# Optimization experiments

Measured on AMD Instinct MI355X. Metric: run time of the kernel, lower is better.

The kernel has to match this reference:

```python
import jax, jax.numpy as jnp
import numpy as np

B, N, H, A, O = 32, 1024, 256, 32, 256
RESAMPLE_THRESHOLD = 0.5
EPS = 1e-10


def setup_inputs() -> dict:
    key = jax.random.key(0)
    ks = jax.random.split(key, 16)
    s = 0.05  # small weight scale (stands in for xavier init, keeps softmax sane)
    w = jax.random.uniform(ks[1], (B, N), jnp.float32)
    return {
        "particles": jax.random.normal(ks[0], (B, N, H), jnp.float32),
        "weights": w / jnp.sum(w, axis=1, keepdims=True),
        "action": jax.random.normal(ks[2], (B, A), jnp.float32),
        "observation": jax.random.normal(ks[3], (B, O), jnp.float32),
        "u": jax.random.uniform(ks[4], (B, 1), jnp.float32),
        "Wr": jax.random.normal(ks[5], (H + A, H), jnp.float32) * s,
        "br": jnp.zeros((H,), jnp.float32),
        "Wu": jax.random.normal(ks[6], (H + A, H), jnp.float32) * s,
        "bu": jnp.zeros((H,), jnp.float32),
        "Wc": jax.random.normal(ks[7], (H + A, H), jnp.float32) * s,
        "bc": jnp.zeros((H,), jnp.float32),
        "W0": jax.random.normal(ks[8], (H + O, H), jnp.float32) * s,
        "b0": jnp.zeros((H,), jnp.float32),
        "W1": jax.random.normal(ks[9], (H, H), jnp.float32) * s,
        "b1": jnp.zeros((H,), jnp.float32),
        "W2": jax.random.normal(ks[10], (H, 1), jnp.float32) * s,
        "b2": jnp.zeros((1,), jnp.float32),
    }


def reference(particles, weights, action, observation, u,
              Wr, br, Wu, bu, Wc, bc, W0, b0, W1, b1, W2, b2):
    b, n, h = particles.shape
    act = jnp.broadcast_to(action[:, None, :], (b, n, action.shape[-1]))
    obs = jnp.broadcast_to(observation[:, None, :], (b, n, observation.shape[-1]))

    # --- GRU-style transition (stochastic head is dead code in update()) ---
    x = jnp.concatenate([particles, act], axis=-1)            # [B,N,H+A]
    reset = jax.nn.sigmoid(x @ Wr + br)
    update = jax.nn.sigmoid(x @ Wu + bu)
    x_reset = jnp.concatenate([particles * reset, act], axis=-1)
    cand = jnp.tanh(x_reset @ Wc + bc)
    nxt = (1.0 - update) * particles + update * cand          # [B,N,H]

    # --- observation log-likelihood MLP ---
    z = jnp.concatenate([nxt, obs], axis=-1)                  # [B,N,H+O]
    z = jax.nn.gelu(z @ W0 + b0, approximate=False)
    z = jax.nn.gelu(z @ W1 + b1, approximate=False)
    log_lik = (z @ W2 + b2)[..., 0]                           # [B,N]

    # --- weight update (stable softmax) ---
    log_w = jnp.log(weights + EPS) + log_lik
    log_w = log_w - jnp.max(log_w, axis=1, keepdims=True)
    new_w = jax.nn.softmax(log_w, axis=1)                     # [B,N]

    ess = 1.0 / (jnp.sum(new_w * new_w, axis=1) + EPS)        # [B]
    should = ess < RESAMPLE_THRESHOLD * n                     # [B] bool

    # --- systematic resampling (computed for all rows, selected by mask) ---
    csum = jnp.cumsum(new_w, axis=1)                          # [B,N]
    pos = u / n + jnp.arange(n, dtype=jnp.float32) / n        # [B,N]
    pos = jnp.minimum(pos, 0.9999)
    idx = jax.vmap(jnp.searchsorted)(csum, pos)               # [B,N]
    idx = jnp.clip(idx, 0, n - 1)
    resampled = jnp.take_along_axis(nxt, idx[..., None], axis=1)
    uniform_w = jnp.full_like(new_w, 1.0 / n)

    nxt = jnp.where(should[:, None, None], resampled, nxt)
    new_w = jnp.where(should[:, None], uniform_w, new_w)

    belief = jnp.sum(nxt * new_w[..., None], axis=1)          # [B,H]
    return belief, nxt, new_w, ess
```

## Files before the change

### kernel.cpp

```cpp
#include <hip/hip_runtime.h>
#include <math.h>

#define B_ 32
#define N_ 1024
#define H_ 256
#define A_ 32
#define O_ 256
#define M_ (B_*N_)
#define EPSF 1e-10f

typedef _Float16 f16;
typedef __attribute__((ext_vector_type(8))) _Float16 f16x8;
typedef __attribute__((ext_vector_type(4))) _Float16 f16x4;
typedef __attribute__((ext_vector_type(2))) _Float16 f16x2;
typedef __attribute__((ext_vector_type(4))) float    f32x4;

__device__ __forceinline__ float gelu_exact(float x){
  return 0.5f * x * (1.0f + erff(x * 0.70710678118654752f));
}
__device__ __forceinline__ float sigm(float x){
  return 1.0f / (1.0f + expf(-x));
}

__global__ __launch_bounds__(256) void k_prep(
    const float* __restrict__ action, const float* __restrict__ observation,
    const float* __restrict__ Wr, const float* __restrict__ br,
    const float* __restrict__ Wu, const float* __restrict__ bu,
    const float* __restrict__ Wc, const float* __restrict__ bc,
    const float* __restrict__ W0, const float* __restrict__ b0,
    f16* __restrict__ WrT, f16* __restrict__ WuT, f16* __restrict__ WcT,
    f16* __restrict__ W0T, f16* __restrict__ W1T, const float* __restrict__ W1,
    float* __restrict__ actR, float* __restrict__ actU,
    float* __restrict__ actC, float* __restrict__ obs0)
{
  const int blk = blockIdx.x;
  if (blk < 80) {
    __shared__ float tile[64][65];
    const int mat = blk >> 4;
    const int kb  = ((blk & 15) >> 2) * 64;
    const int nb  = (blk & 3) * 64;
    const float* W; f16* WT;
    switch (mat) {
      case 0: W = Wr; WT = WrT; break;
      case 1: W = Wu; WT = WuT; break;
      case 2: W = Wc; WT = WcT; break;
      case 3: W = W0; WT = W0T; break;
      default: W = W1; WT = W1T; break;
    }
    const int t = threadIdx.x;
    const int c = t & 63, r4 = t >> 6;
    #pragma unroll
    for (int i = 0; i < 64; i += 4)
      tile[i + r4][c] = W[(size_t)(kb + i + r4)*H_ + nb + c];
    __syncthreads();
    #pragma unroll
    for (int i = 0; i < 64; i += 4)
      WT[(size_t)(nb + i + r4)*H_ + kb + c] = (f16)tile[c][i + r4];
  } else {
    const int b = blk - 80, j = threadIdx.x;
    float aR = br[j], aU = bu[j], aC = bc[j];
    for (int a = 0; a < A_; ++a) {
      float av = action[b*A_ + a];
      aR = fmaf(av, Wr[(H_+a)*H_ + j], aR);
      aU = fmaf(av, Wu[(H_+a)*H_ + j], aU);
      aC = fmaf(av, Wc[(H_+a)*H_ + j], aC);
    }
    float o0 = b0[j];
    for (int o = 0; o < O_; ++o)
      o0 = fmaf(observation[b*O_ + o], W0[(H_+o)*H_ + j], o0);
    actR[b*H_+j] = aR; actU[b*H_+j] = aU; actC[b*H_+j] = aC; obs0[b*H_+j] = o0;
  }
}

__device__ __forceinline__ f16x8 lda(const unsigned char* xs, int m, int kt,
                                     int lr, int lg) {
  int row = m*16 + lr;
  int off = (row*512 + kt*64 + lg*16) ^ ((row&7)<<4);
  return *(const f16x8*)(xs + off);
}
__device__ __forceinline__ f16 xs_r16(const unsigned char* xs, int row, int col) {
  int off = (row*512 + col*2) ^ ((row&7)<<4);
  return *(const f16*)(xs + off);
}
__device__ __forceinline__ void xs_w16(unsigned char* xs, int row, int col, f16 v) {
  int off = (row*512 + col*2) ^ ((row&7)<<4);
  *(f16*)(xs + off) = v;
}

__device__ __forceinline__ void gemm256(const unsigned char* xs, const f16* __restrict__ Wt,
                                        int lr, int lg, int colbase,
                                        f32x4 acc[4][4]) {
  for (int kt = 0; kt < 8; ++kt) {
    f16x8 a[4];
    #pragma unroll
    for (int m = 0; m < 4; ++m) a[m] = lda(xs, m, kt, lr, lg);
    #pragma unroll
    for (int n = 0; n < 4; ++n) {
      f16x8 bb = *(const f16x8*)(Wt + (size_t)(colbase + n*16 + lr)*H_ + kt*32 + lg*8);
      #pragma unroll
      for (int m = 0; m < 4; ++m)
        acc[m][n] = __builtin_amdgcn_mfma_f32_16x16x32_f16(a[m], bb, acc[m][n], 0, 0, 0);
    }
  }
}

__global__ __launch_bounds__(256, 2) void k_gru_mlp(
    const float* __restrict__ particles, const float* __restrict__ weights,
    const f16* __restrict__ WrT, const f16* __restrict__ WuT,
    const f16* __restrict__ WcT, const f16* __restrict__ W0T,
    const f16* __restrict__ W1T,
    const float* __restrict__ W2, const float* __restrict__ b1v,
    const float* __restrict__ b2v,
    const float* __restrict__ actR, const float* __restrict__ actU,
    const float* __restrict__ actC, const float* __restrict__ obs0,
    f16* __restrict__ ws_nxt16, float* __restrict__ log_w)
{
  __shared__ __align__(16) unsigned char xs[64*512];
  __shared__ float red[4][64];

  const int b    = blockIdx.x >> 4;
  const int n0   = (blockIdx.x & 15) << 6;
  const int tid  = threadIdx.x;
  const int w    = tid >> 6;
  const int lane = tid & 63;
  const int lr   = lane & 15;
  const int lg   = lane >> 4;
  const int colbase = w << 6;
  const float* Pbase = particles + (size_t)(b*N_ + n0) * H_;

  int colv[4];
  #pragma unroll
  for (int n = 0; n < 4; ++n) colv[n] = colbase + n*16 + lr;

  #pragma unroll
  for (int i = 0; i < 8; ++i) {
    int s = tid + i*256;
    int row = s >> 5, ks = s & 31;
    const float* src = Pbase + row*H_ + ks*8;
    float4 v0 = *(const float4*)src;
    float4 v1 = *(const float4*)(src + 4);
    f16x8 h;
    h[0]=(f16)v0.x; h[1]=(f16)v0.y; h[2]=(f16)v0.z; h[3]=(f16)v0.w;
    h[4]=(f16)v1.x; h[5]=(f16)v1.y; h[6]=(f16)v1.z; h[7]=(f16)v1.w;
    int off = (row*512 + ks*16) ^ ((row&7)<<4);
    *(f16x8*)(xs + off) = h;
  }
  __syncthreads();

  f32x4 aR[4][4];
  #pragma unroll
  for (int m=0;m<4;++m)
    #pragma unroll
    for (int n=0;n<4;++n) aR[m][n] = (f32x4)(0.f);
  gemm256(xs, WrT, lr, lg, colbase, aR);

  f32x4 aU[4][4];
  #pragma unroll
  for (int m=0;m<4;++m)
    #pragma unroll
    for (int n=0;n<4;++n) aU[m][n] = (f32x4)(0.f);
  gemm256(xs, WuT, lr, lg, colbase, aU);

  float vR[4], vU[4];
  #pragma unroll
  for (int n=0;n<4;++n) { vR[n] = actR[b*H_ + colv[n]]; vU[n] = actU[b*H_ + colv[n]]; }

  f16x4 uh[4][4];
  #pragma unroll
  for (int m=0;m<4;++m)
    #pragma unroll
    for (int n=0;n<4;++n)
      #pragma unroll
      for (int r=0;r<4;++r) {
        aR[m][n][r] = sigm(aR[m][n][r] + vR[n]);
        uh[m][n][r] = (f16)sigm(aU[m][n][r] + vU[n]);
      }

  __syncthreads();

  f16x4 oh[4][4];
  #pragma unroll
  for (int m=0;m<4;++m)
    #pragma unroll
    for (int n=0;n<4;++n)
      #pragma unroll
      for (int r=0;r<4;++r) {
        int row = m*16 + lg*4 + r;
        f16 o = xs_r16(xs, row, colv[n]);
        oh[m][n][r] = o;
        xs_w16(xs, row, colv[n], (f16)((float)o * aR[m][n][r]));
      }
  __syncthreads();

  f32x4 aC[4][4];
  #pragma unroll
  for (int m=0;m<4;++m)
    #pragma unroll
    for (int n=0;n<4;++n) aC[m][n] = (f32x4)(0.f);
  gemm256(xs, WcT, lr, lg, colbase, aC);

  float vC[4];
  #pragma unroll
  for (int n=0;n<4;++n) vC[n] = actC[b*H_ + colv[n]];

  __syncthreads();
  #pragma unroll
  for (int m=0;m<4;++m)
    #pragma unroll
    for (int n=0;n<4;++n)
      #pragma unroll
      for (int r=0;r<4;++r) {
        int row = m*16 + lg*4 + r;
        float cand = tanhf(aC[m][n][r] + vC[n]);
        float orig = (float)oh[m][n][r];
        float nx   = fmaf((float)uh[m][n][r], cand - orig, orig);
        xs_w16(xs, row, colv[n], (f16)nx);
      }
  __syncthreads();

  f16* wsrow = ws_nxt16 + (size_t)(b*N_ + n0) * H_;
  #pragma unroll
  for (int i = 0; i < 8; ++i) {
    int s = tid + i*256;
    int row = s >> 5, c16 = s & 31;
    int off = (row*512 + c16*16) ^ ((row&7)<<4);
    f16x8 v = *(const f16x8*)(xs + off);
    *(f16x8*)(wsrow + row*H_ + c16*8) = v;
  }

  f32x4 a0[4][4];
  #pragma unroll
  for (int m=0;m<4;++m)
    #pragma unroll
    for (int n=0;n<4;++n) a0[m][n] = (f32x4)(0.f);
  gemm256(xs, W0T, lr, lg, colbase, a0);

  float v0b[4];
  #pragma unroll
  for (int n=0;n<4;++n) v0b[n] = obs0[b*H_ + colv[n]];
  #pragma unroll
  for (int m=0;m<4;++m)
    #pragma unroll
    for (int n=0;n<4;++n)
      #pragma unroll
      for (int r=0;r<4;++r)
        a0[m][n][r] = gelu_exact(a0[m][n][r] + v0b[n]);
  __syncthreads();
  #pragma unroll
  for (int m=0;m<4;++m)
    #pragma unroll
    for (int n=0;n<4;++n)
      #pragma unroll
      for (int r=0;r<4;++r)
        xs_w16(xs, m*16 + lg*4 + r, colv[n], (f16)a0[m][n][r]);
  __syncthreads();

  f32x4 a1[4][4];
  #pragma unroll
  for (int m=0;m<4;++m)
    #pragma unroll
    for (int n=0;n<4;++n) a1[m][n] = (f32x4)(0.f);
  gemm256(xs, W1T, lr, lg, colbase, a1);

  float v1b[4], w2v[4];
  #pragma unroll
  for (int n=0;n<4;++n) { v1b[n] = b1v[colv[n]]; w2v[n] = W2[colv[n]]; }

  float psum[4][4];
  #pragma unroll
  for (int m=0;m<4;++m)
    #pragma unroll
    for (int r=0;r<4;++r) psum[m][r] = 0.f;
  #pragma unroll
  for (int m=0;m<4;++m)
    #pragma unroll
    for (int n=0;n<4;++n)
      #pragma unroll
      for (int r=0;r<4;++r)
        psum[m][r] = fmaf(gelu_exact(a1[m][n][r] + v1b[n]), w2v[n], psum[m][r]);

  #pragma unroll
  for (int m=0;m<4;++m)
    #pragma unroll
    for (int r=0;r<4;++r) {
      float v = psum[m][r];
      v += __shfl_xor(v, 1); v += __shfl_xor(v, 2);
      v += __shfl_xor(v, 4); v += __shfl_xor(v, 8);
      psum[m][r] = v;
    }
  if (lr == 0) {
    #pragma unroll
    for (int m=0;m<4;++m)
      #pragma unroll
      for (int r=0;r<4;++r)
        red[w][m*16 + lg*4 + r] = psum[m][r];
  }
  __syncthreads();
  if (tid < 64) {
    float ll = red[0][tid] + red[1][tid] + red[2][tid] + red[3][tid] + b2v[0];
    int gi = b*N_ + n0 + tid;
    log_w[gi] = logf(weights[gi] + EPSF) + ll;
  }
}

__global__ __launch_bounds__(256) void k_softmax(
    const float* __restrict__ log_w, const float* __restrict__ u_in,
    float* __restrict__ d_new_w, float* __restrict__ d_ess,
    int* __restrict__ ws_idx, float* __restrict__ ws_should)
{
  __shared__ float cs[N_];
  __shared__ float redbuf[4];
  __shared__ float wsum[4];
  const int b = blockIdx.x, t = threadIdx.x;
  const int wave = t >> 6, lane = t & 63;
  const float* lw = log_w + b*N_;

  float v[4];
  float m = -INFINITY;
  #pragma unroll
  for (int q = 0; q < 4; ++q) { v[q] = lw[t*4+q]; m = fmaxf(m, v[q]); }
  for (int off = 32; off >= 1; off >>= 1) m = fmaxf(m, __shfl_xor(m, off));
  if (lane == 0) redbuf[wave] = m;
  __syncthreads();
  m = fmaxf(fmaxf(redbuf[0], redbuf[1]), fmaxf(redbuf[2], redbuf[3]));

  float s4 = 0.f;
  #pragma unroll
  for (int q = 0; q < 4; ++q) { v[q] = expf(v[q] - m); s4 += v[q]; }

  float incl = s4;
  #pragma unroll
  for (int off = 1; off < 64; off <<= 1) {
    float t2 = __shfl_up(incl, off);
    if (lane >= off) incl += t2;
  }
  if (lane == 63) wsum[wave] = incl;
  __syncthreads();
  float woff = 0.f;
  #pragma unroll
  for (int ww = 0; ww < 4; ++ww) woff += (ww < wave) ? wsum[ww] : 0.f;
  const float total = wsum[0] + wsum[1] + wsum[2] + wsum[3];
  const float excl  = woff + incl - s4;
  const float inv   = 1.0f / total;

  float run = excl, sq4 = 0.f;
  #pragma unroll
  for (int q = 0; q < 4; ++q) {
    run += v[q];
    cs[t*4+q] = run * inv;
    float wq = v[q] * inv;
    sq4 += wq * wq;
  }
  for (int off = 32; off >= 1; off >>= 1) sq4 += __shfl_xor(sq4, off);
  __syncthreads();
  if (lane == 0) redbuf[wave] = sq4;
  __syncthreads();
  const float ssq = redbuf[0] + redbuf[1] + redbuf[2] + redbuf[3];
  const float ess = 1.0f / (ssq + EPSF);
  const bool should = ess < (0.5f * (float)N_);
  if (t == 0) { d_ess[b] = ess; ws_should[b] = should ? 1.0f : 0.0f; }

  const float uw = 1.0f / (float)N_;
  #pragma unroll
  for (int q = 0; q < 4; ++q)
    d_new_w[b*N_ + t*4+q] = should ? uw : v[q] * inv;

  const float ub = u_in[b];
  #pragma unroll
  for (int q = 0; q < 4; ++q) {
    int i = t*4 + q;
    float pos = fminf(ub / (float)N_ + (float)i / (float)N_, 0.9999f);
    int lo = 0, hi = N_;
    while (lo < hi) { int mid = (lo + hi) >> 1; if (cs[mid] < pos) lo = mid + 1; else hi = mid; }
    ws_idx[b*N_ + i] = (lo < N_-1) ? lo : N_-1;
  }
}

__global__ __launch_bounds__(256) void k_final(
    const f16* __restrict__ ws_nxt16, const int* __restrict__ ws_idx,
    const float* __restrict__ ws_should, const float* __restrict__ d_new_w,
    float* __restrict__ d_nxt, float* __restrict__ d_belief)
{
  const int blk = blockIdx.x;
  const int b   = blk >> 4;
  const int n0  = (blk & 15) << 6;
  const int t   = threadIdx.x;
  const int c   = t & 127;
  const int hf  = t >> 7;
  const bool should = ws_should[b] != 0.0f;
  float p0 = 0.f, p1 = 0.f;
  #pragma unroll 4
  for (int r = 0; r < 32; ++r) {
    int n = n0 + hf*32 + r;
    int src = should ? ws_idx[b*N_ + n] : n;
    f16x2 v = *(const f16x2*)(ws_nxt16 + (size_t)(b*N_ + src)*H_ + c*2);
    float w = d_new_w[b*N_ + n];
    float2 st; st.x = (float)v[0]; st.y = (float)v[1];
    *(float2*)(d_nxt + (size_t)(b*N_ + n)*H_ + c*2) = st;
    p0 = fmaf(st.x, w, p0); p1 = fmaf(st.y, w, p1);
  }
  atomicAdd(&d_belief[b*H_ + c*2],     p0);
  atomicAdd(&d_belief[b*H_ + c*2 + 1], p1);
}

extern "C" void kernel_launch(void* const* d_in, const int* in_sizes, int n_in,
                              void* d_out, int out_size, void* d_ws, size_t ws_size,
                              hipStream_t stream) {
  (void)in_sizes; (void)n_in; (void)out_size; (void)ws_size;
  const float* particles   = (const float*)d_in[0];
  const float* weights     = (const float*)d_in[1];
  const float* action      = (const float*)d_in[2];
  const float* observation = (const float*)d_in[3];
  const float* u_in        = (const float*)d_in[4];
  const float* Wr = (const float*)d_in[5];
  const float* br = (const float*)d_in[6];
  const float* Wu = (const float*)d_in[7];
  const float* bu = (const float*)d_in[8];
  const float* Wc = (const float*)d_in[9];
  const float* bc = (const float*)d_in[10];
  const float* W0 = (const float*)d_in[11];
  const float* b0 = (const float*)d_in[12];
  const float* W1 = (const float*)d_in[13];
  const float* b1 = (const float*)d_in[14];
  const float* W2 = (const float*)d_in[15];
  const float* b2 = (const float*)d_in[16];

  float* out      = (float*)d_out;
  float* d_belief = out;
  float* d_nxt    = out + (size_t)B_*H_;
  float* d_new_w  = d_nxt + (size_t)M_*H_;
  float* d_ess    = d_new_w + M_;

  unsigned char* wsb = (unsigned char*)d_ws;
  f16* WrT = (f16*)wsb;
  f16* WuT = WrT + H_*H_;
  f16* WcT = WuT + H_*H_;
  f16* W0T = WcT + H_*H_;
  f16* W1T = W0T + H_*H_;
  f16* ws_nxt16   = W1T + H_*H_;
  float* ws_logw  = (float*)(ws_nxt16 + (size_t)M_*H_);
  float* ws_actR  = ws_logw + M_;
  float* ws_actU  = ws_actR + B_*H_;
  float* ws_actC  = ws_actU + B_*H_;
  float* ws_obs0  = ws_actC + B_*H_;
  int*   ws_idx   = (int*)(ws_obs0 + B_*H_);
  float* ws_should= (float*)(ws_idx + M_);

  hipMemsetAsync(d_belief, 0, (size_t)B_*H_*sizeof(float), stream);

  k_prep<<<dim3(112), dim3(256), 0, stream>>>(
      action, observation, Wr, br, Wu, bu, Wc, bc, W0, b0,
      WrT, WuT, WcT, W0T, W1T, W1,
      ws_actR, ws_actU, ws_actC, ws_obs0);

  k_gru_mlp<<<dim3(M_/64), dim3(256), 0, stream>>>(
      particles, weights, WrT, WuT, WcT, W0T, W1T, W2, b1, b2,
      ws_actR, ws_actU, ws_actC, ws_obs0, ws_nxt16, ws_logw);

  k_softmax<<<dim3(B_), dim3(256), 0, stream>>>(
      ws_logw, u_in, d_new_w, d_ess, ws_idx, ws_should);

  k_final<<<dim3(M_/64), dim3(256), 0, stream>>>(
      ws_nxt16, ws_idx, ws_should, d_new_w, d_nxt, d_belief);
}
```

Baseline: 270.2 us.

## Double-buffer LDS tiles to cut live accumulators and barriers in GRU-MLP kernel

Adds a second 32KB LDS buffer so the original particle tile stays in xs2 while the reset-gated tile is written to xs. The reset gate is now applied right after its GEMM, which reuses one accumulator array in place of holding aR, aU, aC and the f16 copy of the original particles at once. This is meant to lower VGPR pressure and remove a couple of __syncthreads. In exchange LDS per block doubles to about 64KB, which may limit how many blocks fit per CU under launch_bounds(256,2).

```diff
diff --git a/kernel.cpp b/kernel.cpp
--- a/kernel.cpp
+++ b/kernel.cpp
@@ -104,6 +104,12 @@
   }
 }
 
+#define ZERO_ACC(acc)                                                          \
+  _Pragma("unroll")                                                            \
+  for (int m=0;m<4;++m)                                                        \
+    _Pragma("unroll")                                                          \
+    for (int n=0;n<4;++n) acc[m][n] = (f32x4)(0.f);
+
 __global__ __launch_bounds__(256, 2) void k_gru_mlp(
     const float* __restrict__ particles, const float* __restrict__ weights,
     const f16* __restrict__ WrT, const f16* __restrict__ WuT,
@@ -115,7 +121,8 @@
     const float* __restrict__ actC, const float* __restrict__ obs0,
     f16* __restrict__ ws_nxt16, float* __restrict__ log_w)
 {
-  __shared__ __align__(16) unsigned char xs[64*512];
+  __shared__ __align__(16) unsigned char xs [64*512];
+  __shared__ __align__(16) unsigned char xs2[64*512];
   __shared__ float red[4][64];
 
   const int b    = blockIdx.x >> 4;
@@ -143,79 +150,69 @@
     h[0]=(f16)v0.x; h[1]=(f16)v0.y; h[2]=(f16)v0.z; h[3]=(f16)v0.w;
     h[4]=(f16)v1.x; h[5]=(f16)v1.y; h[6]=(f16)v1.z; h[7]=(f16)v1.w;
     int off = (row*512 + ks*16) ^ ((row&7)<<4);
-    *(f16x8*)(xs + off) = h;
-  }
-  __syncthreads();
-
-  f32x4 aR[4][4];
-  #pragma unroll
-  for (int m=0;m<4;++m)
-    #pragma unroll
-    for (int n=0;n<4;++n) aR[m][n] = (f32x4)(0.f);
-  gemm256(xs, WrT, lr, lg, colbase, aR);
-
-  f32x4 aU[4][4];
-  #pragma unroll
-  for (int m=0;m<4;++m)
-    #pragma unroll
-    for (int n=0;n<4;++n) aU[m][n] = (f32x4)(0.f);
-  gemm256(xs, WuT, lr, lg, colbase, aU);
-
-  float vR[4], vU[4];
-  #pragma unroll
-  for (int n=0;n<4;++n) { vR[n] = actR[b*H_ + colv[n]]; vU[n] = actU[b*H_ + colv[n]]; }
-
+    *(f16x8*)(xs2 + off) = h;
+  }
+  __syncthreads();
+
+  f32x4 acc[4][4];
+
+  ZERO_ACC(acc);
+  gemm256(xs2, WrT, lr, lg, colbase, acc);
+  {
+    float vR[4];
+    #pragma unroll
+    for (int n=0;n<4;++n) vR[n] = actR[b*H_ + colv[n]];
+    #pragma unroll
+    for (int m=0;m<4;++m)
+      #pragma unroll
+      for (int n=0;n<4;++n)
+        #pragma unroll
+        for (int r=0;r<4;++r) {
+          int row = m*16 + lg*4 + r;
+          float Rv = sigm(acc[m][n][r] + vR[n]);
+          float o  = (float)xs_r16(xs2, row, colv[n]);
+          xs_w16(xs, row, colv[n], (f16)(o * Rv));
+        }
+  }
+  __syncthreads();
+
+  ZERO_ACC(acc);
+  gemm256(xs2, WuT, lr, lg, colbase, acc);
   f16x4 uh[4][4];
-  #pragma unroll
-  for (int m=0;m<4;++m)
-    #pragma unroll
-    for (int n=0;n<4;++n)
-      #pragma unroll
-      for (int r=0;r<4;++r) {
-        aR[m][n][r] = sigm(aR[m][n][r] + vR[n]);
-        uh[m][n][r] = (f16)sigm(aU[m][n][r] + vU[n]);
-      }
-
-  __syncthreads();
-
-  f16x4 oh[4][4];
-  #pragma unroll
-  for (int m=0;m<4;++m)
-    #pragma unroll
-    for (int n=0;n<4;++n)
-      #pragma unroll
-      for (int r=0;r<4;++r) {
-        int row = m*16 + lg*4 + r;
-        f16 o = xs_r16(xs, row, colv[n]);
-        oh[m][n][r] = o;
-        xs_w16(xs, row, colv[n], (f16)((float)o * aR[m][n][r]));
-      }
-  __syncthreads();
-
-  f32x4 aC[4][4];
-  #pragma unroll
-  for (int m=0;m<4;++m)
-    #pragma unroll
-    for (int n=0;n<4;++n) aC[m][n] = (f32x4)(0.f);
-  gemm256(xs, WcT, lr, lg, colbase, aC);
-
-  float vC[4];
-  #pragma unroll
-  for (int n=0;n<4;++n) vC[n] = actC[b*H_ + colv[n]];
-
-  __syncthreads();
-  #pragma unroll
-  for (int m=0;m<4;++m)
-    #pragma unroll
-    for (int n=0;n<4;++n)
-      #pragma unroll
-      for (int r=0;r<4;++r) {
-        int row = m*16 + lg*4 + r;
-        float cand = tanhf(aC[m][n][r] + vC[n]);
-        float orig = (float)oh[m][n][r];
-        float nx   = fmaf((float)uh[m][n][r], cand - orig, orig);
-        xs_w16(xs, row, colv[n], (f16)nx);
-      }
+  {
+    float vU[4];
+    #pragma unroll
+    for (int n=0;n<4;++n) vU[n] = actU[b*H_ + colv[n]];
+    #pragma unroll
+    for (int m=0;m<4;++m)
+      #pragma unroll
+      for (int n=0;n<4;++n)
+        #pragma unroll
+        for (int r=0;r<4;++r)
+          uh[m][n][r] = (f16)sigm(acc[m][n][r] + vU[n]);
+  }
+
+  ZERO_ACC(acc);
+  gemm256(xs, WcT, lr, lg, colbase, acc);
+  __syncthreads();
+
+  {
+    float vC[4];
+    #pragma unroll
+    for (int n=0;n<4;++n) vC[n] = actC[b*H_ + colv[n]];
+    #pragma unroll
+    for (int m=0;m<4;++m)
+      #pragma unroll
+      for (int n=0;n<4;++n)
+        #pragma unroll
+        for (int r=0;r<4;++r) {
+          int row = m*16 + lg*4 + r;
+          float cand = tanhf(acc[m][n][r] + vC[n]);
+          float o    = (float)xs_r16(xs2, row, colv[n]);
+          float nx   = fmaf((float)uh[m][n][r], cand - o, o);
+          xs_w16(xs2, row, colv[n], (f16)nx);
+        }
+  }
   __syncthreads();
 
   f16* wsrow = ws_nxt16 + (size_t)(b*N_ + n0) * H_;
@@ -224,60 +221,46 @@
     int s = tid + i*256;
     int row = s >> 5, c16 = s & 31;
     int off = (row*512 + c16*16) ^ ((row&7)<<4);
-    f16x8 v = *(const f16x8*)(xs + off);
+    f16x8 v = *(const f16x8*)(xs2 + off);
     *(f16x8*)(wsrow + row*H_ + c16*8) = v;
   }
 
-  f32x4 a0[4][4];
+  ZERO_ACC(acc);
+  gemm256(xs2, W0T, lr, lg, colbase, acc);
+  {
+    float v0b[4];
+    #pragma unroll
+    for (int n=0;n<4;++n) v0b[n] = obs0[b*H_ + colv[n]];
+    #pragma unroll
+    for (int m=0;m<4;++m)
+      #pragma unroll
+      for (int n=0;n<4;++n)
+        #pragma unroll
+        for (int r=0;r<4;++r)
+          xs_w16(xs, m*16 + lg*4 + r, colv[n],
+                 (f16)gelu_exact(acc[m][n][r] + v0b[n]));
+  }
+  __syncthreads();
+
+  ZERO_ACC(acc);
+  gemm256(xs, W1T, lr, lg, colbase, acc);
+
+  float v1b[4], w2v[4];
+  #pragma unroll
+  for (int n=0;n<4;++n) { v1b[n] = b1v[colv[n]]; w2v[n] = W2[colv[n]]; }
+
+  float psum[4][4];
   #pragma unroll
   for (int m=0;m<4;++m)
     #pragma unroll
-    for (int n=0;n<4;++n) a0[m][n] = (f32x4)(0.f);
-  gemm256(xs, W0T, lr, lg, colbase, a0);
-
-  float v0b[4];
-  #pragma unroll
-  for (int n=0;n<4;++n) v0b[n] = obs0[b*H_ + colv[n]];
+    for (int r=0;r<4;++r) psum[m][r] = 0.f;
   #pragma unroll
   for (int m=0;m<4;++m)
     #pragma unroll
     for (int n=0;n<4;++n)
       #pragma unroll
       for (int r=0;r<4;++r)
-        a0[m][n][r] = gelu_exact(a0[m][n][r] + v0b[n]);
-  __syncthreads();
-  #pragma unroll
-  for (int m=0;m<4;++m)
-    #pragma unroll
-    for (int n=0;n<4;++n)
-      #pragma unroll
-      for (int r=0;r<4;++r)
-        xs_w16(xs, m*16 + lg*4 + r, colv[n], (f16)a0[m][n][r]);
-  __syncthreads();
-
-  f32x4 a1[4][4];
-  #pragma unroll
-  for (int m=0;m<4;++m)
-    #pragma unroll
-    for (int n=0;n<4;++n) a1[m][n] = (f32x4)(0.f);
-  gemm256(xs, W1T, lr, lg, colbase, a1);
-
-  float v1b[4], w2v[4];
-  #pragma unroll
-  for (int n=0;n<4;++n) { v1b[n] = b1v[colv[n]]; w2v[n] = W2[colv[n]]; }
-
-  float psum[4][4];
-  #pragma unroll
-  for (int m=0;m<4;++m)
-    #pragma unroll
-    for (int r=0;r<4;++r) psum[m][r] = 0.f;
-  #pragma unroll
-  for (int m=0;m<4;++m)
-    #pragma unroll
-    for (int n=0;n<4;++n)
-      #pragma unroll
-      for (int r=0;r<4;++r)
-        psum[m][r] = fmaf(gelu_exact(a1[m][n][r] + v1b[n]), w2v[n], psum[m][r]);
+        psum[m][r] = fmaf(gelu_exact(acc[m][n][r] + v1b[n]), w2v[n], psum[m][r]);
 
   #pragma unroll
   for (int m=0;m<4;++m)
```

New measurement: 230.4 us. -14.8%, faster.
